# Kernel tuning notes

Hardware: AMD Instinct MI355X
Metric: run time of the kernel (lower is better)

## Reference

```python
import jax, jax.numpy as jnp
import numpy as np

B, T, D = 4, 4000, 1024
H = 8
DK = D // H          # key dim per head; value dim per head also DK (value_factor=1)
CHUNK = 500
EPS_LN = 1e-5
EPS_RMS = 1e-6


def rotate_every_two(x):
    x1 = x[..., ::2]
    x2 = x[..., 1::2]
    return jnp.stack((-x2, x1), axis=-1).reshape(x.shape)


def theta_shift(x, sin, cos):
    # x: [b,h,t,dk]; sin/cos: [t,dk]
    return x * cos + rotate_every_two(x) * sin


def rel_pos(slen, chunk_len, num_heads, key_dim):
    # RetNetRelPos(chunkwise_recurrent=True)
    angle = 1.0 / (10000 ** jnp.linspace(0.0, 1.0, key_dim // 2))
    angle = jnp.repeat(angle, 2)  # == unsqueeze(-1).repeat(1,2).flatten()
    decay = jnp.log(1.0 - 2.0 ** (-5.0 - jnp.arange(num_heads, dtype=jnp.float32)))
    index = jnp.arange(slen, dtype=jnp.float32)
    sin = jnp.sin(index[:, None] * angle[None, :])  # [t,dk]
    cos = jnp.cos(index[:, None] * angle[None, :])
    bi = jnp.arange(chunk_len, dtype=jnp.float32)
    tril = jnp.tril(jnp.ones((chunk_len, chunk_len), bool))
    diff = bi[:, None] - bi[None, :]
    mask = jnp.where(tril[None], jnp.exp(decay[:, None, None] * diff[None]), 0.0)  # [H,C,C]
    last_row = mask[:, -1]                                            # [H,C]
    value_inner_decay = (last_row / last_row.sum(-1, keepdims=True))[:, :, None]  # [H,C,1]
    scale = jnp.sqrt(mask.sum(-1, keepdims=True))                     # [H,C,1]
    inner_mask = mask / scale
    cross_decay = jnp.exp(decay * chunk_len)[:, None, None]           # [H,1,1]
    qid = jnp.exp(decay[:, None] * (bi + 1.0))[:, :, None]            # [H,C,1]
    query_inner_decay = qid / (scale / last_row.sum(-1)[:, None, None])
    return (sin, cos), (inner_mask, cross_decay, query_inner_decay, value_inner_decay)


def retention_chunkwise(qr, kr, v, inner):
    mask, cross_decay, query_inner_decay, value_inner_decay = inner
    b, t = v.shape[0], v.shape[1]
    C = mask.shape[1]
    n = t // C
    h, dk = qr.shape[1], qr.shape[3]
    dv = v.shape[2] // h
    # [b,h,t,dk] -> [b,n,h,C,dk]
    qr = qr.transpose(0, 2, 1, 3).reshape(b, n, C, h, dk).transpose(0, 1, 3, 2, 4)
    kr = kr.transpose(0, 2, 1, 3).reshape(b, n, C, h, dk).transpose(0, 1, 3, 2, 4)
    v = v.reshape(b, n, C, h, dv).transpose(0, 1, 3, 2, 4)  # [b,n,h,C,dv]

    qk = jnp.einsum('bnhcd,bnhed->bnhce', qr, kr) * mask  # [b,n,h,C,C]
    inner_scale = jnp.clip(jnp.abs(jax.lax.stop_gradient(qk)).sum(-1, keepdims=True), 1.0, None)
    qk = qk / inner_scale
    inner_output = jnp.einsum('bnhce,bnhed->bnhcd', qk, v)  # [b,n,h,C,dv]

    kv = jnp.einsum('bnhck,bnhcv->bnhkv', kr, v * value_inner_decay)  # [b,n,h,dk,dv]

    def step(carry, kv_i):
        kv_state, kv_scale = carry
        out = (kv_state / kv_scale, kv_scale)
        new_state = kv_state * cross_decay + kv_i
        sg = jnp.abs(jax.lax.stop_gradient(new_state)).sum(-2, keepdims=True).max(-1, keepdims=True)
        return (new_state, jnp.clip(sg, 1.0, None)), out

    init = (jnp.zeros((b, h, dk, dv), v.dtype), jnp.ones((b, h, 1, 1), v.dtype))
    _, (kv_rec, cross_scale) = jax.lax.scan(step, init, jnp.moveaxis(kv, 1, 0))
    kv_rec = jnp.moveaxis(kv_rec, 0, 1)            # [b,n,h,dk,dv]
    cross_scale = jnp.moveaxis(cross_scale, 0, 1)  # [b,n,h,1,1]

    all_scale = jnp.maximum(inner_scale, cross_scale)
    cross_output = jnp.einsum('bnhcd,bnhdv->bnhcv', qr * query_inner_decay, kv_rec)
    output = inner_output / (all_scale / inner_scale) + cross_output / (all_scale / cross_scale)
    return output.transpose(0, 1, 3, 2, 4).reshape(b, t, h, dv)  # [b,t,h,dv]


def setup_inputs() -> dict:
    key = jax.random.key(0)
    ks = jax.random.split(key, 6)
    s = 0.02
    return {
        'inputs': jax.random.normal(ks[0], (B, T, D), jnp.float32),
        'ln_gamma': jnp.ones((D,), jnp.float32),
        'ln_beta': jnp.zeros((D,), jnp.float32),
        'Wq': jax.random.normal(ks[1], (D, D), jnp.float32) * s,
        'Wk': jax.random.normal(ks[2], (D, D), jnp.float32) * s,
        'Wv': jax.random.normal(ks[3], (D, D), jnp.float32) * s,
        'Wg': jax.random.normal(ks[4], (D, D), jnp.float32) * s,
        'Wo': jax.random.normal(ks[5], (D, D), jnp.float32) * s,
    }


def reference(inputs, ln_gamma, ln_beta, Wq, Wk, Wv, Wg, Wo):
    b, t, d = inputs.shape
    # pre-LayerNorm
    mu = inputs.mean(-1, keepdims=True)
    var = ((inputs - mu) ** 2).mean(-1, keepdims=True)
    x = (inputs - mu) / jnp.sqrt(var + EPS_LN) * ln_gamma + ln_beta

    (sin, cos), inner = rel_pos(t, CHUNK, H, DK)

    q = (x @ Wq).reshape(b, t, H, DK).transpose(0, 2, 1, 3)
    k = (x @ Wk * (DK ** -0.5)).reshape(b, t, H, DK).transpose(0, 2, 1, 3)
    v = x @ Wv
    g = x @ Wg

    qr = theta_shift(q, sin, cos)
    kr = theta_shift(k, sin, cos)

    out = retention_chunkwise(qr, kr, v, inner)  # [b,t,H,dv]
    # group norm: per-head RMSNorm without affine
    out = out * jax.lax.rsqrt(jnp.mean(out ** 2, -1, keepdims=True) + EPS_RMS)
    out = out.reshape(b, t, H * DK)
    out = jax.nn.silu(g) * out
    return out @ Wo  # dropout is identity in eval
```

## Files before the change

### kernel.cpp

```cpp
#include <hip/hip_runtime.h>
#include <hip/hip_bf16.h>


typedef __attribute__((ext_vector_type(4))) float f32x4;
typedef __attribute__((ext_vector_type(8))) short s16x8;

#define DEV static __device__ __forceinline__

DEV float bfu(ushort u){ union{uint i; float f;} x; x.i=((uint)u)<<16; return x.f; }
DEV float bflo(uint w){ union{uint i; float f;} x; x.i=w<<16; return x.f; }
DEV float bfhi(uint w){ union{uint i; float f;} x; x.i=w&0xffff0000u; return x.f; }
DEV ushort f2bf(float f){ union{float f; uint u;} x; x.f=f; uint r = x.u + 0x7fffu + ((x.u>>16)&1u); return (ushort)(r>>16); }
DEV uint pack2(float lo, float hi){ return ((uint)f2bf(hi)<<16) | (uint)f2bf(lo); }
DEV void unpack8(uint4 u, float* f){
  f[0]=bflo(u.x); f[1]=bfhi(u.x); f[2]=bflo(u.y); f[3]=bfhi(u.y);
  f[4]=bflo(u.z); f[5]=bfhi(u.z); f[6]=bflo(u.w); f[7]=bfhi(u.w);
}
DEV void cstore(float* C, size_t i, float v){ C[i]=v; }
DEV void cstore(ushort* C, size_t i, float v){ C[i]=f2bf(v); }

DEV void gload16(const ushort* g, ushort* l) {
  __builtin_amdgcn_global_load_lds((const __attribute__((address_space(1))) void*)g,
                                   (__attribute__((address_space(3))) void*)l, 16, 0, 0);
}

__global__ __launch_bounds__(256) void f2bf_t_kernel(const float* __restrict__ src,
                                                     ushort* __restrict__ dst) {
  __shared__ ushort t[64][72];
  int kt = blockIdx.x*64, nt = blockIdx.y*64;
  int tid = threadIdx.x;
  int r = tid>>2, c0 = (tid&3)*16;
  const float* s = src + (size_t)(kt+r)*1024 + nt + c0;
  #pragma unroll
  for (int j=0;j<16;j+=4) {
    float4 vv = *(const float4*)(s+j);
    t[r][c0+j]=f2bf(vv.x); t[r][c0+j+1]=f2bf(vv.y); t[r][c0+j+2]=f2bf(vv.z); t[r][c0+j+3]=f2bf(vv.w);
  }
  __syncthreads();
  union { uint4 u4[2]; ushort s16[16]; } tmp;
  #pragma unroll
  for (int j=0;j<16;j++) tmp.s16[j] = t[c0+j][r];
  ushort* d = dst + (size_t)(nt+r)*1024 + kt + c0;
  *(uint4*)(d)   = tmp.u4[0];
  *(uint4*)(d+8) = tmp.u4[1];
}

__global__ __launch_bounds__(256) void ln_kernel(const float* __restrict__ x,
                                                 const float* __restrict__ gamma,
                                                 const float* __restrict__ beta,
                                                 ushort* __restrict__ xo) {
  int row = blockIdx.x;
  int tid = threadIdx.x;
  const float* xr = x + (size_t)row*1024;
  float4 u = ((const float4*)xr)[tid];
  float s = u.x+u.y+u.z+u.w;
  float sq = u.x*u.x+u.y*u.y+u.z*u.z+u.w*u.w;
  #pragma unroll
  for (int o=32;o;o>>=1){ s += __shfl_xor(s,o); sq += __shfl_xor(sq,o); }
  __shared__ float red[8];
  int wv=tid>>6, ln=tid&63;
  if (ln==0){ red[wv]=s; red[4+wv]=sq; }
  __syncthreads();
  s = red[0]+red[1]+red[2]+red[3];
  sq = red[4]+red[5]+red[6]+red[7];
  float mu = s*(1.0f/1024.0f);
  float var = sq*(1.0f/1024.0f)-mu*mu;
  float inv = rsqrtf(var+1e-5f);
  float4 gg = ((const float4*)gamma)[tid];
  float4 bb = ((const float4*)beta)[tid];
  float o0=(u.x-mu)*inv*gg.x+bb.x;
  float o1=(u.y-mu)*inv*gg.y+bb.y;
  float o2=(u.z-mu)*inv*gg.z+bb.z;
  float o3=(u.w-mu)*inv*gg.w+bb.w;
  uint2 w; w.x=pack2(o0,o1); w.y=pack2(o2,o3);
  ((uint2*)(xo+(size_t)row*1024))[tid]=w;
}

__global__ __launch_bounds__(256) void sincos_kernel(float* __restrict__ sint, float* __restrict__ cost) {
  int idx = blockIdx.x*256+threadIdx.x;
  if (idx >= 4000*64) return;
  int t = idx>>6, i = idx&63;
  float ang = expf(-9.210340371976184f * (float)i * (1.0f/63.0f));
  float a = (float)t * ang;
  float sv = sinf(a), cv = cosf(a);
  sint[(size_t)t*128+2*i] = sv; sint[(size_t)t*128+2*i+1] = sv;
  cost[(size_t)t*128+2*i] = cv; cost[(size_t)t*128+2*i+1] = cv;
}

template<typename OutT>
__global__ __launch_bounds__(256) void gemm_bt(const ushort* __restrict__ A,
                                               const ushort* __restrict__ BT,
                                               OutT* __restrict__ C,
                                               int M, int N, int K) {
  __shared__ ushort As[128*32];
  __shared__ ushort Bs[128*32];
  int ny = N>>7;
  int cpx = ((M>>7)*ny)>>3;
  int wg = blockIdx.x;
  int orig = (wg&7)*cpx + (wg>>3);
  int bm = (orig>>3)*128, bn = (orig&7)*128;
  int tid = threadIdx.x;
  int w = tid>>6, l = tid&63;
  int wm = (w>>1)*64, wn = (w&1)*64;
  int rsel = l&15, ko = (l>>4)*8;
  f32x4 acc[4][4];
  #pragma unroll
  for (int i=0;i<4;i++)
    #pragma unroll
    for (int j=0;j<4;j++){ acc[i][j][0]=0; acc[i][j][1]=0; acc[i][j][2]=0; acc[i][j][3]=0; }
  const ushort* ap0 = A  + (size_t)(bm + w*32 + (l>>2))*K + (l&3)*8;
  const ushort* ap1 = ap0 + (size_t)16*K;
  const ushort* bp0 = BT + (size_t)(bn + w*32 + (l>>2))*K + (l&3)*8;
  const ushort* bp1 = bp0 + (size_t)16*K;
  ushort* abase = As + w*1024;
  ushort* bbase = Bs + w*1024;
  for (int kt=0; kt<K; kt+=32) {
    __syncthreads();
    gload16(ap0+kt, abase);
    gload16(ap1+kt, abase+512);
    gload16(bp0+kt, bbase);
    gload16(bp1+kt, bbase+512);
    __syncthreads();
    s16x8 af[4], bfr[4];
    #pragma unroll
    for (int mf=0;mf<4;mf++) af[mf]  = *(const s16x8*)&As[(wm+mf*16+rsel)*32 + ko];
    #pragma unroll
    for (int nf=0;nf<4;nf++) bfr[nf] = *(const s16x8*)&Bs[(wn+nf*16+rsel)*32 + ko];
    #pragma unroll
    for (int mf=0;mf<4;mf++)
      #pragma unroll
      for (int nf=0;nf<4;nf++)
        acc[mf][nf] = __builtin_amdgcn_mfma_f32_16x16x32_bf16(af[mf], bfr[nf], acc[mf][nf], 0,0,0);
  }
  int crow = bm+wm+(l>>4)*4;
  int ccol = bn+wn+(l&15);
  #pragma unroll
  for (int mf=0;mf<4;mf++)
    #pragma unroll
    for (int nf=0;nf<4;nf++)
      #pragma unroll
      for (int r2=0;r2<4;r2++)
        cstore(C, (size_t)(crow+mf*16+r2)*N + ccol+nf*16, acc[mf][nf][r2]);
}

__global__ __launch_bounds__(256) void rotary_kernel(ushort* __restrict__ q, ushort* __restrict__ k,
                                                     const float* __restrict__ sint,
                                                     const float* __restrict__ cost) {
  int idx = blockIdx.x*256+threadIdx.x;
  if (idx >= 16000*512) return;
  int row = idx>>9, cp = idx&511;
  int col = cp*2;
  int t = row - (row/4000)*4000;
  int d = col & 127;
  float c = cost[(size_t)t*128+d], s = sint[(size_t)t*128+d];
  uint* qp = (uint*)(q + (size_t)row*1024 + col);
  uint w = *qp;
  float q0=bflo(w), q1=bfhi(w);
  *qp = pack2(q0*c - q1*s, q1*c + q0*s);
  uint* kp = (uint*)(k + (size_t)row*1024 + col);
  w = *kp;
  float k0=bflo(w), k1=bfhi(w);
  const float sc = 0.08838834764831845f;
  *kp = pack2((k0*c - k1*s)*sc, (k1*c + k0*s)*sc);
}

__global__ __launch_bounds__(256) void kv_mfma(const ushort* __restrict__ kr,
                                               const ushort* __restrict__ v,
                                               float* __restrict__ kvp) {
  int bnh = blockIdx.x, half = blockIdx.y;
  int h = bnh&7, n=(bnh>>3)&7, b=bnh>>6;
  size_t base = (size_t)(b*4000+n*500)*1024 + h*128;
  float Dh = 1.0f - exp2f(-5.0f-(float)h);
  float decay = logf(Dh);
  float ls = (1.0f - expf(decay*500.0f))/(1.0f-Dh);
  float inv_ls = 1.0f/ls;
  __shared__ ushort kT[128*72];
  __shared__ ushort vT[128*72];
  int tid=threadIdx.x;
  int wv=tid>>6, l=tid&63, g=l>>4, c16=l&15;
  int srow=tid>>2, sc0=(tid&3)*32;
  int cbeg = half*250, cend = cbeg+250;
  f32x4 acc[2][8];
  #pragma unroll
  for (int i=0;i<2;i++)
    #pragma unroll
    for (int j=0;j<8;j++){ acc[i][j][0]=0; acc[i][j][1]=0; acc[i][j][2]=0; acc[i][j][3]=0; }
  for (int ct=cbeg; ct<cend; ct+=64) {
    if (ct!=cbeg) __syncthreads();
    int c = ct + srow;
    int cc = min(c, 499);
    const ushort* ks = kr + base + (size_t)cc*1024 + sc0;
    const ushort* vs = v  + base + (size_t)cc*1024 + sc0;
    float vid = (c < cend && c < 500) ? expf(decay*(float)(499-c))*inv_ls : 0.0f;
    #pragma unroll
    for (int j=0;j<4;j++) {
      union{uint4 u; ushort s[8];} tk; tk.u = *(const uint4*)(ks+j*8);
      uint4 vv = *(const uint4*)(vs+j*8);
      float vf[8]; unpack8(vv,vf);
      #pragma unroll
      for (int x=0;x<8;x++) {
        kT[(sc0+j*8+x)*72 + srow] = tk.s[x];
        vT[(sc0+j*8+x)*72 + srow] = f2bf(vf[x]*vid);
      }
    }
    __syncthreads();
    #pragma unroll
    for (int kc=0;kc<2;kc++) {
      s16x8 a0 = *(const s16x8*)&kT[(wv*32 +      c16)*72 + kc*32 + g*8];
      s16x8 a1 = *(const s16x8*)&kT[(wv*32 + 16 + c16)*72 + kc*32 + g*8];
      #pragma unroll
      for (int nf=0;nf<8;nf++) {
        s16x8 bb = *(const s16x8*)&vT[(nf*16 + c16)*72 + kc*32 + g*8];
        acc[0][nf] = __builtin_amdgcn_mfma_f32_16x16x32_bf16(a0, bb, acc[0][nf], 0,0,0);
        acc[1][nf] = __builtin_amdgcn_mfma_f32_16x16x32_bf16(a1, bb, acc[1][nf], 0,0,0);
      }
    }
  }
  float* outp = kvp + ((size_t)half*256 + bnh)*16384;
  #pragma unroll
  for (int mf=0;mf<2;mf++)
    #pragma unroll
    for (int nf=0;nf<8;nf++)
      #pragma unroll
      for (int reg=0;reg<4;reg++)
        outp[(size_t)(wv*32 + mf*16 + g*4 + reg)*128 + nf*16 + c16] = acc[mf][nf][reg];
}

__global__ __launch_bounds__(256) void scan_kernel(const float* __restrict__ kvp,
                                                   ushort* __restrict__ kvrecT,
                                                   float* __restrict__ crosssc) {
  int bh = blockIdx.x;
  int b = bh>>3, h = bh&7;
  float Dh = 1.0f - exp2f(-5.0f-(float)h);
  float decay = logf(Dh);
  float cd = expf(decay*500.0f);
  int tid=threadIdx.x;
  int vcol = tid&127, khalf = tid>>7;
  float st[64];
  #pragma unroll
  for (int i=0;i<64;i++) st[i]=0;
  float scale = 1.0f;
  __shared__ float colpart[2][128];
  __shared__ float sred[2];
  for (int n=0;n<8;n++) {
    int bnh = (b*8+n)*8+h;
    const float* s0 = kvp + (size_t)bnh*16384;
    const float* s1 = kvp + (size_t)(256+bnh)*16384;
    ushort* rec = kvrecT + (size_t)bnh*16384;
    float inv = 1.0f/scale;
    float cs = 0;
    #pragma unroll
    for (int i=0;i<64;i++) {
      int kk = khalf*64+i;
      rec[(size_t)vcol*128+kk] = f2bf(st[i]*inv);
      st[i] = st[i]*cd + s0[(size_t)kk*128+vcol] + s1[(size_t)kk*128+vcol];
      cs += fabsf(st[i]);
    }
    if (tid==0) crosssc[bnh] = scale;
    colpart[khalf][vcol] = cs;
    __syncthreads();
    if (tid<128) colpart[0][tid] += colpart[1][tid];
    __syncthreads();
    float m = (tid<128)? colpart[0][tid] : 0.0f;
    #pragma unroll
    for (int o=32;o;o>>=1) m = fmaxf(m,__shfl_xor(m,o));
    if (tid<128 && (tid&63)==0) sred[tid>>6]=m;
    __syncthreads();
    scale = fmaxf(fmaxf(sred[0],sred[1]),1.0f);
    __syncthreads();
  }
}

__global__ __launch_bounds__(256) void iout_mfma(const ushort* __restrict__ qr,
                                                 const ushort* __restrict__ kr,
                                                 const ushort* __restrict__ v,
                                                 const ushort* __restrict__ kvrecT,
                                                 const float* __restrict__ crosssc,
                                                 ushort* __restrict__ O) {
  int bnh = blockIdx.x, rt = blockIdx.y;
  int h = bnh&7, n=(bnh>>3)&7, b=bnh>>6;
  size_t base = (size_t)(b*4000+n*500)*1024 + h*128;
  float Dh = 1.0f - exp2f(-5.0f-(float)h);
  float decay = logf(Dh);

  __shared__ ushort sh[31232];
  ushort* qt = sh;
  ushort* kt = sh + 8704;
  ushort* vt = sh + 17408;
  ushort* pt = sh + 26624;
  ushort* kvt = sh + 8704;

  int tid = threadIdx.x;
  int wv = tid>>6, l = tid&63;
  int g = l>>4, c16 = l&15;
  int srow = tid>>2, sc0 = (tid&3)*32;

  {
    int gq = rt*64+srow; if (gq>499) gq=499;
    const ushort* src = qr + base + (size_t)gq*1024 + sc0;
    #pragma unroll
    for (int j=0;j<4;j++) *(uint4*)&qt[srow*136 + sc0 + j*8] = *(const uint4*)(src + j*8);
  }
  int r_base = rt*64 + wv*16 + g*4;
  float er[4];
  #pragma unroll
  for (int reg=0;reg<4;reg++) er[reg] = expf(decay*(float)(r_base+reg));

  f32x4 pv[8], cc[8];
  #pragma unroll
  for (int i=0;i<8;i++){
    #pragma unroll
    for (int j=0;j<4;j++){ pv[i][j]=0.0f; cc[i][j]=0.0f; }
  }
  float rowsum[4] = {0,0,0,0};
  __syncthreads();

  for (int et=0; et<=rt; et++) {
    if (et) __syncthreads();
    {
      int ge = et*64+srow; if (ge>499) ge=499;
      const ushort* ks = kr + base + (size_t)ge*1024 + sc0;
      const ushort* vs = v  + base + (size_t)ge*1024 + sc0;
      #pragma unroll
      for (int j=0;j<4;j++) {
        *(uint4*)&kt[srow*136 + sc0 + j*8] = *(const uint4*)(ks + j*8);
        union{uint4 u; ushort s[8];} tv; tv.u = *(const uint4*)(vs + j*8);
        #pragma unroll
        for (int x=0;x<8;x++) vt[(sc0+j*8+x)*72 + srow] = tv.s[x];
      }
    }
    __syncthreads();
    f32x4 S[4];
    #pragma unroll
    for (int i=0;i<4;i++){ S[i][0]=0; S[i][1]=0; S[i][2]=0; S[i][3]=0; }
    #pragma unroll
    for (int kc=0;kc<4;kc++) {
      s16x8 a = *(const s16x8*)&qt[(wv*16 + c16)*136 + kc*32 + g*8];
      #pragma unroll
      for (int ni=0;ni<4;ni++) {
        s16x8 bf2 = *(const s16x8*)&kt[(ni*16 + c16)*136 + kc*32 + g*8];
        S[ni] = __builtin_amdgcn_mfma_f32_16x16x32_bf16(a, bf2, S[ni], 0,0,0);
      }
    }
    #pragma unroll
    for (int ni=0;ni<4;ni++) {
      int e_rel = et*64 + ni*16 + c16;
      float ie = expf(-decay*(float)e_rel);
      #pragma unroll
      for (int reg=0;reg<4;reg++) {
        int rr = r_base + reg;
        float p = (e_rel <= rr) ? S[ni][reg]*er[reg]*ie : 0.0f;
        rowsum[reg] += fabsf(p);
        pt[(wv*16 + g*4 + reg)*72 + ni*16 + c16] = f2bf(p);
      }
    }
    #pragma unroll
    for (int kc=0;kc<2;kc++) {
      s16x8 pa = *(const s16x8*)&pt[(wv*16 + c16)*72 + kc*32 + g*8];
      #pragma unroll
      for (int nf=0;nf<8;nf++) {
        s16x8 vb = *(const s16x8*)&vt[(nf*16 + c16)*72 + kc*32 + g*8];
        pv[nf] = __builtin_amdgcn_mfma_f32_16x16x32_bf16(pa, vb, pv[nf], 0,0,0);
      }
    }
  }
  #pragma unroll
  for (int reg=0;reg<4;reg++) {
    float s = rowsum[reg];
    s += __shfl_xor(s,1); s += __shfl_xor(s,2); s += __shfl_xor(s,4); s += __shfl_xor(s,8);
    rowsum[reg] = s;
  }
  __syncthreads();
  {
    int r2 = tid>>1, c0 = (tid&1)*64;
    const ushort* src = kvrecT + (size_t)bnh*16384 + (size_t)r2*128 + c0;
    #pragma unroll
    for (int j=0;j<8;j++) *(uint4*)&kvt[r2*136 + c0 + j*8] = *(const uint4*)(src + j*8);
  }
  __syncthreads();
  #pragma unroll
  for (int kc=0;kc<4;kc++) {
    s16x8 a = *(const s16x8*)&qt[(wv*16 + c16)*136 + kc*32 + g*8];
    #pragma unroll
    for (int nf=0;nf<8;nf++) {
      s16x8 bb = *(const s16x8*)&kvt[(nf*16 + c16)*136 + kc*32 + g*8];
      cc[nf] = __builtin_amdgcn_mfma_f32_16x16x32_bf16(a, bb, cc[nf], 0,0,0);
    }
  }
  float cs = crosssc[bnh];
  float lsum = (1.0f-expf(decay*500.0f))/(1.0f-Dh);
  #pragma unroll
  for (int reg=0;reg<4;reg++) {
    int rr = r_base + reg;
    if (rr < 500) {
      float rs = (1.0f-expf(decay*(float)(rr+1)))/(1.0f-Dh);
      float rsr = rsqrtf(rs);
      float is = fmaxf(1.0f, rowsum[reg]*rsr);
      float all = fmaxf(is, cs);
      float qid = expf(decay*(float)(rr+1))*lsum*rsr;
      float fi = rsr/all;
      float fc = qid*(cs/all);
      ushort* dst = O + (size_t)(b*4000+n*500+rr)*1024 + h*128;
      #pragma unroll
      for (int nf=0;nf<8;nf++)
        dst[nf*16 + c16] = f2bf(pv[nf][reg]*fi + cc[nf][reg]*fc);
    }
  }
}

__global__ __launch_bounds__(256) void rms_silu_kernel(const ushort* __restrict__ O,
                                                       const ushort* __restrict__ g,
                                                       ushort* __restrict__ op) {
  int row = blockIdx.x, tid=threadIdx.x;
  int wave=tid>>6, lane=tid&63;
  const ushort* Orow = O + (size_t)row*1024;
  const ushort* grow = g + (size_t)row*1024;
  ushort* orow = op + (size_t)row*1024;
  for (int hh=0; hh<2; hh++) {
    int h = wave*2+hh;
    int c0 = h*128+lane, c1=c0+64;
    float a = bfu(Orow[c0]), b2 = bfu(Orow[c1]);
    float ss = a*a+b2*b2;
    #pragma unroll
    for (int o=32;o;o>>=1) ss += __shfl_xor(ss,o);
    float sc = rsqrtf(ss*(1.0f/128.0f)+1e-6f);
    float g0=bfu(grow[c0]), g1=bfu(grow[c1]);
    float s0 = g0/(1.0f+expf(-g0)), s1 = g1/(1.0f+expf(-g1));
    orow[c0] = f2bf(s0*a*sc);
    orow[c1] = f2bf(s1*b2*sc);
  }
}

extern "C" void kernel_launch(void* const* d_in, const int* in_sizes, int n_in,
                              void* d_out, int out_size, void* d_ws, size_t ws_size,
                              hipStream_t stream) {
  const float* x     = (const float*)d_in[0];
  const float* gamma = (const float*)d_in[1];
  const float* beta  = (const float*)d_in[2];
  const float* Wq    = (const float*)d_in[3];
  const float* Wk    = (const float*)d_in[4];
  const float* Wv    = (const float*)d_in[5];
  const float* Wg    = (const float*)d_in[6];
  const float* Wo    = (const float*)d_in[7];
  float* out = (float*)d_out;

  char* ws = (char*)d_ws;
  size_t off = 0;
  auto alloc = [&](size_t bytes)->void* { void* p = ws+off; off += (bytes+255)&~(size_t)255; return p; };
  const size_t BT1024 = (size_t)16000*1024;
  ushort* xln  = (ushort*)alloc(BT1024*2);
  ushort* q    = (ushort*)alloc(BT1024*2);
  ushort* k    = (ushort*)alloc(BT1024*2);
  ushort* v    = (ushort*)alloc(BT1024*2);
  ushort* g    = (ushort*)alloc(BT1024*2);
  ushort* O    = (ushort*)alloc(BT1024*2);
  ushort* WqT  = (ushort*)alloc((size_t)1024*1024*2);
  ushort* WkT  = (ushort*)alloc((size_t)1024*1024*2);
  ushort* WvT  = (ushort*)alloc((size_t)1024*1024*2);
  ushort* WgT  = (ushort*)alloc((size_t)1024*1024*2);
  ushort* WoT  = (ushort*)alloc((size_t)1024*1024*2);
  float* sint  = (float*)alloc((size_t)4000*128*4);
  float* cost  = (float*)alloc((size_t)4000*128*4);
  float* kvp   = (float*)alloc((size_t)512*16384*4);
  ushort* kvrecT=(ushort*)alloc((size_t)256*16384*2);
  float* crosssc = (float*)alloc(256*4);
  (void)ws_size; (void)in_sizes; (void)n_in; (void)out_size;

  ln_kernel<<<16000,256,0,stream>>>(x,gamma,beta,xln);
  sincos_kernel<<<1000,256,0,stream>>>(sint,cost);
  dim3 tt(16,16);
  f2bf_t_kernel<<<tt,256,0,stream>>>(Wq,WqT);
  f2bf_t_kernel<<<tt,256,0,stream>>>(Wk,WkT);
  f2bf_t_kernel<<<tt,256,0,stream>>>(Wv,WvT);
  f2bf_t_kernel<<<tt,256,0,stream>>>(Wg,WgT);
  f2bf_t_kernel<<<tt,256,0,stream>>>(Wo,WoT);

  gemm_bt<ushort><<<1000,256,0,stream>>>(xln,WqT,q,16000,1024,1024);
  gemm_bt<ushort><<<1000,256,0,stream>>>(xln,WkT,k,16000,1024,1024);
  gemm_bt<ushort><<<1000,256,0,stream>>>(xln,WvT,v,16000,1024,1024);
  gemm_bt<ushort><<<1000,256,0,stream>>>(xln,WgT,g,16000,1024,1024);

  rotary_kernel<<<32000,256,0,stream>>>(q,k,sint,cost);

  dim3 gkv(256,2);
  kv_mfma<<<gkv,256,0,stream>>>(k,v,kvp);
  scan_kernel<<<32,256,0,stream>>>(kvp,kvrecT,crosssc);

  dim3 gr(256,8);
  iout_mfma<<<gr,256,0,stream>>>(q,k,v,kvrecT,crosssc,O);

  ushort* opre = xln;
  rms_silu_kernel<<<16000,256,0,stream>>>(O,g,opre);
  gemm_bt<float><<<1000,256,0,stream>>>(opre,WoT,out,16000,1024,1024);
}
```

Before: 471.4 us.

## Double-buffer GEMM, pre-transpose K/V, fold decays into q/k, fuse RMS+SiLU

Several changes land together. The projection GEMM now double-buffers its LDS tiles so the next K-slice loads while MFMAs run. Rotary for K moves into a new kernel that also folds the per-position decay into q and k and writes transposed K/V copies. kv_mfma and iout_mfma use those copies through swizzled LDS loaded with global_load_lds. The RMSNorm and SiLU gating move into the retention output epilogue, which removes the O buffer and the separate rms_silu pass. Folding the decay as exp(-decay*c) into k can lose precision for large in-chunk offsets with bf16 storage.

Measured after the change: 478.6 us. No clear change (+1.5%).

```diff
diff --git a/kernel.cpp b/kernel.cpp
--- a/kernel.cpp
+++ b/kernel.cpp
@@ -92,8 +92,8 @@
                                                const ushort* __restrict__ BT,
                                                OutT* __restrict__ C,
                                                int M, int N, int K) {
-  __shared__ ushort As[128*32];
-  __shared__ ushort Bs[128*32];
+  __shared__ ushort As[8192];
+  __shared__ ushort Bs[8192];
   int ny = N>>7;
   int cpx = ((M>>7)*ny)>>3;
   int wg = blockIdx.x;
@@ -112,25 +112,33 @@
   const ushort* ap1 = ap0 + (size_t)16*K;
   const ushort* bp0 = BT + (size_t)(bn + w*32 + (l>>2))*K + (l&3)*8;
   const ushort* bp1 = bp0 + (size_t)16*K;
-  ushort* abase = As + w*1024;
-  ushort* bbase = Bs + w*1024;
+  {
+    ushort* ab = As + w*1024; ushort* bb = Bs + w*1024;
+    gload16(ap0, ab); gload16(ap1, ab+512);
+    gload16(bp0, bb); gload16(bp1, bb+512);
+  }
+  int cur = 0;
   for (int kt=0; kt<K; kt+=32) {
     __syncthreads();
-    gload16(ap0+kt, abase);
-    gload16(ap1+kt, abase+512);
-    gload16(bp0+kt, bbase);
-    gload16(bp1+kt, bbase+512);
-    __syncthreads();
+    if (kt+32 < K) {
+      int nb = cur^1;
+      ushort* ab = As + nb*4096 + w*1024; ushort* bb = Bs + nb*4096 + w*1024;
+      gload16(ap0+kt+32, ab); gload16(ap1+kt+32, ab+512);
+      gload16(bp0+kt+32, bb); gload16(bp1+kt+32, bb+512);
+    }
+    const ushort* Ac = As + cur*4096;
+    const ushort* Bc = Bs + cur*4096;
     s16x8 af[4], bfr[4];
     #pragma unroll
-    for (int mf=0;mf<4;mf++) af[mf]  = *(const s16x8*)&As[(wm+mf*16+rsel)*32 + ko];
-    #pragma unroll
-    for (int nf=0;nf<4;nf++) bfr[nf] = *(const s16x8*)&Bs[(wn+nf*16+rsel)*32 + ko];
+    for (int mf=0;mf<4;mf++) af[mf]  = *(const s16x8*)&Ac[(wm+mf*16+rsel)*32 + ko];
+    #pragma unroll
+    for (int nf=0;nf<4;nf++) bfr[nf] = *(const s16x8*)&Bc[(wn+nf*16+rsel)*32 + ko];
     #pragma unroll
     for (int mf=0;mf<4;mf++)
       #pragma unroll
       for (int nf=0;nf<4;nf++)
         acc[mf][nf] = __builtin_amdgcn_mfma_f32_16x16x32_bf16(af[mf], bfr[nf], acc[mf][nf], 0,0,0);
+    cur ^= 1;
   }
   int crow = bm+wm+(l>>4)*4;
   int ccol = bn+wn+(l&15);
@@ -143,87 +151,138 @@
         cstore(C, (size_t)(crow+mf*16+r2)*N + ccol+nf*16, acc[mf][nf][r2]);
 }
 
-__global__ __launch_bounds__(256) void rotary_kernel(ushort* __restrict__ q, ushort* __restrict__ k,
-                                                     const float* __restrict__ sint,
-                                                     const float* __restrict__ cost) {
+__global__ __launch_bounds__(256) void qrot_kernel(ushort* __restrict__ q,
+                                                   const float* __restrict__ sint,
+                                                   const float* __restrict__ cost) {
   int idx = blockIdx.x*256+threadIdx.x;
   if (idx >= 16000*512) return;
   int row = idx>>9, cp = idx&511;
   int col = cp*2;
   int t = row - (row/4000)*4000;
-  int d = col & 127;
+  int d = col & 127, h = col>>7;
+  int r_rel = t - (t/500)*500;
+  float decay = logf(1.0f - exp2f(-5.0f-(float)h));
+  float qs = expf(decay*(float)r_rel);
   float c = cost[(size_t)t*128+d], s = sint[(size_t)t*128+d];
   uint* qp = (uint*)(q + (size_t)row*1024 + col);
   uint w = *qp;
   float q0=bflo(w), q1=bfhi(w);
-  *qp = pack2(q0*c - q1*s, q1*c + q0*s);
-  uint* kp = (uint*)(k + (size_t)row*1024 + col);
-  w = *kp;
-  float k0=bflo(w), k1=bfhi(w);
-  const float sc = 0.08838834764831845f;
-  *kp = pack2((k0*c - k1*s)*sc, (k1*c + k0*s)*sc);
-}
-
-__global__ __launch_bounds__(256) void kv_mfma(const ushort* __restrict__ kr,
-                                               const ushort* __restrict__ v,
-                                               float* __restrict__ kvp) {
-  int bnh = blockIdx.x, half = blockIdx.y;
+  *qp = pack2((q0*c - q1*s)*qs, (q1*c + q0*s)*qs);
+}
+
+__global__ __launch_bounds__(256) void kvT_kernel(ushort* __restrict__ k,
+                                                  const ushort* __restrict__ v,
+                                                  ushort* __restrict__ kT,
+                                                  ushort* __restrict__ vT,
+                                                  const float* __restrict__ sint,
+                                                  const float* __restrict__ cost) {
+  int bnh = blockIdx.x, ct = blockIdx.y;
   int h = bnh&7, n=(bnh>>3)&7, b=bnh>>6;
   size_t base = (size_t)(b*4000+n*500)*1024 + h*128;
-  float Dh = 1.0f - exp2f(-5.0f-(float)h);
-  float decay = logf(Dh);
-  float ls = (1.0f - expf(decay*500.0f))/(1.0f-Dh);
-  float inv_ls = 1.0f/ls;
-  __shared__ ushort kT[128*72];
-  __shared__ ushort vT[128*72];
+  float decay = logf(1.0f - exp2f(-5.0f-(float)h));
+  __shared__ ushort ktl[64][136];
+  __shared__ ushort vtl[64][136];
+  int tid = threadIdx.x;
+  int srow = tid>>2, sc0 = (tid&3)*32;
+  int c = ct*64 + srow;
+  if (c < 500) {
+    int t = n*500 + c;
+    float ksc = expf(-decay*(float)c) * 0.08838834764831845f;
+    ushort* kp = k + base + (size_t)c*1024 + sc0;
+    const ushort* vp = v + base + (size_t)c*1024 + sc0;
+    #pragma unroll
+    for (int j=0;j<4;j++) {
+      uint4 kw = *(const uint4*)(kp+j*8);
+      float kf[8]; unpack8(kw,kf);
+      uint4 ko4;
+      uint* kou = (uint*)&ko4;
+      #pragma unroll
+      for (int p=0;p<4;p++) {
+        int d = sc0+j*8+2*p;
+        float cc = cost[(size_t)t*128+d], ss = sint[(size_t)t*128+d];
+        float r0 = (kf[2*p]*cc - kf[2*p+1]*ss)*ksc;
+        float r1 = (kf[2*p+1]*cc + kf[2*p]*ss)*ksc;
+        kou[p] = pack2(r0,r1);
+      }
+      *(uint4*)&ktl[srow][sc0+j*8] = ko4;
+      *(uint4*)(kp+j*8) = ko4;
+      *(uint4*)&vtl[srow][sc0+j*8] = *(const uint4*)(vp+j*8);
+    }
+  } else {
+    uint4 z; z.x=0;z.y=0;z.z=0;z.w=0;
+    #pragma unroll
+    for (int j=0;j<4;j++){ *(uint4*)&ktl[srow][sc0+j*8]=z; *(uint4*)&vtl[srow][sc0+j*8]=z; }
+  }
+  __syncthreads();
+  int d = tid>>1, ch = (tid&1)*32;
+  union{uint4 u4[4]; ushort s[32];} pk, pv_;
+  #pragma unroll
+  for (int j=0;j<32;j++){ pk.s[j] = ktl[ch+j][d]; pv_.s[j] = vtl[ch+j][d]; }
+  ushort* kd = kT + (size_t)bnh*65536 + (size_t)d*512 + ct*64 + ch;
+  ushort* vd = vT + (size_t)bnh*65536 + (size_t)d*512 + ct*64 + ch;
+  #pragma unroll
+  for (int j=0;j<4;j++){ *(uint4*)(kd+j*8) = pk.u4[j]; *(uint4*)(vd+j*8) = pv_.u4[j]; }
+}
+
+__global__ __launch_bounds__(256) void kv_mfma(const ushort* __restrict__ kT,
+                                               const ushort* __restrict__ vT,
+                                               float* __restrict__ kvp) {
+  int bnh = blockIdx.x;
+  __shared__ ushort sh2[16384];
   int tid=threadIdx.x;
   int wv=tid>>6, l=tid&63, g=l>>4, c16=l&15;
-  int srow=tid>>2, sc0=(tid&3)*32;
-  int cbeg = half*250, cend = cbeg+250;
-  f32x4 acc[2][8];
-  #pragma unroll
-  for (int i=0;i<2;i++)
-    #pragma unroll
-    for (int j=0;j<8;j++){ acc[i][j][0]=0; acc[i][j][1]=0; acc[i][j][2]=0; acc[i][j][3]=0; }
-  for (int ct=cbeg; ct<cend; ct+=64) {
-    if (ct!=cbeg) __syncthreads();
-    int c = ct + srow;
-    int cc = min(c, 499);
-    const ushort* ks = kr + base + (size_t)cc*1024 + sc0;
-    const ushort* vs = v  + base + (size_t)cc*1024 + sc0;
-    float vid = (c < cend && c < 500) ? expf(decay*(float)(499-c))*inv_ls : 0.0f;
-    #pragma unroll
-    for (int j=0;j<4;j++) {
-      union{uint4 u; ushort s[8];} tk; tk.u = *(const uint4*)(ks+j*8);
-      uint4 vv = *(const uint4*)(vs+j*8);
-      float vf[8]; unpack8(vv,vf);
-      #pragma unroll
-      for (int x=0;x<8;x++) {
-        kT[(sc0+j*8+x)*72 + srow] = tk.s[x];
-        vT[(sc0+j*8+x)*72 + srow] = f2bf(vf[x]*vid);
-      }
+  int wr = wv>>1, wc = wv&1;
+  int ri[4], ro[4];
+  #pragma unroll
+  for (int jj=0;jj<4;jj++){
+    int i = wv*256 + jj*64 + l;
+    ri[jj] = i>>3;
+    ro[jj] = (((i&7)*16) ^ ((ri[jj]&7)<<4))>>1;
+  }
+  const ushort* kbase = kT + (size_t)bnh*65536;
+  const ushort* vbase = vT + (size_t)bnh*65536;
+  f32x4 acc[4][4];
+  #pragma unroll
+  for (int i=0;i<4;i++)
+    #pragma unroll
+    for (int j=0;j<4;j++){ acc[i][j][0]=0; acc[i][j][1]=0; acc[i][j][2]=0; acc[i][j][3]=0; }
+  for (int ctep=0; ctep<8; ctep++) {
+    int cb = ctep*64;
+    __syncthreads();
+    #pragma unroll
+    for (int jj=0;jj<4;jj++){
+      gload16(kbase + (size_t)ri[jj]*512 + cb + ro[jj], (ushort*)((char*)sh2 + wv*4096 + jj*1024));
+      gload16(vbase + (size_t)ri[jj]*512 + cb + ro[jj], (ushort*)((char*)sh2 + 16384 + wv*4096 + jj*1024));
     }
     __syncthreads();
     #pragma unroll
     for (int kc=0;kc<2;kc++) {
-      s16x8 a0 = *(const s16x8*)&kT[(wv*32 +      c16)*72 + kc*32 + g*8];
-      s16x8 a1 = *(const s16x8*)&kT[(wv*32 + 16 + c16)*72 + kc*32 + g*8];
-      #pragma unroll
-      for (int nf=0;nf<8;nf++) {
-        s16x8 bb = *(const s16x8*)&vT[(nf*16 + c16)*72 + kc*32 + g*8];
-        acc[0][nf] = __builtin_amdgcn_mfma_f32_16x16x32_bf16(a0, bb, acc[0][nf], 0,0,0);
-        acc[1][nf] = __builtin_amdgcn_mfma_f32_16x16x32_bf16(a1, bb, acc[1][nf], 0,0,0);
-      }
-    }
-  }
-  float* outp = kvp + ((size_t)half*256 + bnh)*16384;
-  #pragma unroll
-  for (int mf=0;mf<2;mf++)
-    #pragma unroll
-    for (int nf=0;nf<8;nf++)
+      s16x8 af[4], bf2[4];
+      #pragma unroll
+      for (int mf=0;mf<4;mf++){
+        int row = wr*64+mf*16+c16;
+        af[mf] = *(const s16x8*)((const char*)sh2 + row*128 + ((((kc*32+g*8)*2)) ^ ((row&7)<<4)));
+      }
+      #pragma unroll
+      for (int nf=0;nf<4;nf++){
+        int row = wc*64+nf*16+c16;
+        bf2[nf] = *(const s16x8*)((const char*)sh2 + 16384 + row*128 + ((((kc*32+g*8)*2)) ^ ((row&7)<<4)));
+      }
+      #pragma unroll
+      for (int mf=0;mf<4;mf++)
+        #pragma unroll
+        for (int nf=0;nf<4;nf++)
+          acc[mf][nf] = __builtin_amdgcn_mfma_f32_16x16x32_bf16(af[mf], bf2[nf], acc[mf][nf], 0,0,0);
+    }
+  }
+  float* outp = kvp + (size_t)bnh*16384;
+  #pragma unroll
+  for (int mf=0;mf<4;mf++)
+    #pragma unroll
+    for (int nf=0;nf<4;nf++)
       #pragma unroll
       for (int reg=0;reg<4;reg++)
-        outp[(size_t)(wv*32 + mf*16 + g*4 + reg)*128 + nf*16 + c16] = acc[mf][nf][reg];
+        outp[(size_t)(wr*64+mf*16+g*4+reg)*128 + wc*64+nf*16+c16] = acc[mf][nf][reg];
 }
 
 __global__ __launch_bounds__(256) void scan_kernel(const float* __restrict__ kvp,
@@ -234,6 +293,8 @@
   float Dh = 1.0f - exp2f(-5.0f-(float)h);
   float decay = logf(Dh);
   float cd = expf(decay*500.0f);
+  float ls = (1.0f - expf(decay*500.0f))/(1.0f-Dh);
+  float cst = expf(decay*499.0f)/ls;
   int tid=threadIdx.x;
   int vcol = tid&127, khalf = tid>>7;
   float st[64];
@@ -244,8 +305,7 @@
   __shared__ float sred[2];
   for (int n=0;n<8;n++) {
     int bnh = (b*8+n)*8+h;
-    const float* s0 = kvp + (size_t)bnh*16384;
-    const float* s1 = kvp + (size_t)(256+bnh)*16384;
+    const float* src = kvp + (size_t)bnh*16384;
     ushort* rec = kvrecT + (size_t)bnh*16384;
     float inv = 1.0f/scale;
     float cs = 0;
@@ -253,7 +313,7 @@
     for (int i=0;i<64;i++) {
       int kk = khalf*64+i;
       rec[(size_t)vcol*128+kk] = f2bf(st[i]*inv);
-      st[i] = st[i]*cd + s0[(size_t)kk*128+vcol] + s1[(size_t)kk*128+vcol];
+      st[i] = st[i]*cd + cst*src[(size_t)kk*128+vcol];
       cs += fabsf(st[i]);
     }
     if (tid==0) crosssc[bnh] = scale;
@@ -271,40 +331,39 @@
   }
 }
 
-__global__ __launch_bounds__(256) void iout_mfma(const ushort* __restrict__ qr,
-                                                 const ushort* __restrict__ kr,
-                                                 const ushort* __restrict__ v,
-                                                 const ushort* __restrict__ kvrecT,
-                                                 const float* __restrict__ crosssc,
-                                                 ushort* __restrict__ O) {
+__global__ __launch_bounds__(256,4) void iout_mfma(const ushort* __restrict__ qr,
+                                                   const ushort* __restrict__ kr,
+                                                   const ushort* __restrict__ vT,
+                                                   const ushort* __restrict__ kvrecT,
+                                                   const float* __restrict__ crosssc,
+                                                   const ushort* __restrict__ gbuf,
+                                                   ushort* __restrict__ opre) {
   int bnh = blockIdx.x, rt = blockIdx.y;
   int h = bnh&7, n=(bnh>>3)&7, b=bnh>>6;
   size_t base = (size_t)(b*4000+n*500)*1024 + h*128;
   float Dh = 1.0f - exp2f(-5.0f-(float)h);
   float decay = logf(Dh);
-
-  __shared__ ushort sh[31232];
-  ushort* qt = sh;
-  ushort* kt = sh + 8704;
-  ushort* vt = sh + 17408;
-  ushort* pt = sh + 26624;
-  ushort* kvt = sh + 8704;
-
+  __shared__ ushort sh[20480];
+  char* shb = (char*)sh;
   int tid = threadIdx.x;
   int wv = tid>>6, l = tid&63;
   int g = l>>4, c16 = l&15;
-  int srow = tid>>2, sc0 = (tid&3)*32;
-
-  {
-    int gq = rt*64+srow; if (gq>499) gq=499;
-    const ushort* src = qr + base + (size_t)gq*1024 + sc0;
-    #pragma unroll
-    for (int j=0;j<4;j++) *(uint4*)&qt[srow*136 + sc0 + j*8] = *(const uint4*)(src + j*8);
-  }
   int r_base = rt*64 + wv*16 + g*4;
-  float er[4];
-  #pragma unroll
-  for (int reg=0;reg<4;reg++) er[reg] = expf(decay*(float)(r_base+reg));
+
+  int qrow = rt*64 + wv*16 + c16; if (qrow>499) qrow=499;
+  s16x8 aq[4];
+  #pragma unroll
+  for (int kc=0;kc<4;kc++)
+    aq[kc] = *(const s16x8*)(qr + base + (size_t)qrow*1024 + kc*32 + g*8);
+
+  int ktrow[4], ktofs[4], vtrow[4], vtofs[4];
+  #pragma unroll
+  for (int jj=0;jj<4;jj++){
+    int i = wv*256 + jj*64 + l;
+    int r_ = i>>4;  ktrow[jj]=r_;  ktofs[jj] = (((i&15)*16) ^ ((r_&7)<<4))>>1;
+    int r2_ = i>>3; vtrow[jj]=r2_; vtofs[jj] = (((i&7)*16) ^ ((r2_&7)<<4))>>1;
+  }
+  const ushort* vTb = vT + (size_t)bnh*65536;
 
   f32x4 pv[8], cc[8];
   #pragma unroll
@@ -313,21 +372,14 @@
     for (int j=0;j<4;j++){ pv[i][j]=0.0f; cc[i][j]=0.0f; }
   }
   float rowsum[4] = {0,0,0,0};
-  __syncthreads();
 
   for (int et=0; et<=rt; et++) {
-    if (et) __syncthreads();
-    {
-      int ge = et*64+srow; if (ge>499) ge=499;
-      const ushort* ks = kr + base + (size_t)ge*1024 + sc0;
-      const ushort* vs = v  + base + (size_t)ge*1024 + sc0;
-      #pragma unroll
-      for (int j=0;j<4;j++) {
-        *(uint4*)&kt[srow*136 + sc0 + j*8] = *(const uint4*)(ks + j*8);
-        union{uint4 u; ushort s[8];} tv; tv.u = *(const uint4*)(vs + j*8);
-        #pragma unroll
-        for (int x=0;x<8;x++) vt[(sc0+j*8+x)*72 + srow] = tv.s[x];
-      }
+    __syncthreads();
+    #pragma unroll
+    for (int jj=0;jj<4;jj++){
+      int gr = et*64 + ktrow[jj]; if (gr>499) gr=499;
+      gload16(kr + base + (size_t)gr*1024 + ktofs[jj], (ushort*)(shb + wv*4096 + jj*1024));
+      gload16(vTb + (size_t)vtrow[jj]*512 + et*64 + vtofs[jj], (ushort*)(shb + 16384 + wv*4096 + jj*1024));
     }
     __syncthreads();
     f32x4 S[4];
@@ -335,31 +387,34 @@
     for (int i=0;i<4;i++){ S[i][0]=0; S[i][1]=0; S[i][2]=0; S[i][3]=0; }
     #pragma unroll
     for (int kc=0;kc<4;kc++) {
-      s16x8 a = *(const s16x8*)&qt[(wv*16 + c16)*136 + kc*32 + g*8];
       #pragma unroll
       for (int ni=0;ni<4;ni++) {
-        s16x8 bf2 = *(const s16x8*)&kt[(ni*16 + c16)*136 + kc*32 + g*8];
-        S[ni] = __builtin_amdgcn_mfma_f32_16x16x32_bf16(a, bf2, S[ni], 0,0,0);
-      }
-    }
+        int krow = ni*16+c16;
+        s16x8 bf = *(const s16x8*)(shb + krow*256 + ((((kc*32+g*8)*2)) ^ ((krow&7)<<4)));
+        S[ni] = __builtin_amdgcn_mfma_f32_16x16x32_bf16(aq[kc], bf, S[ni], 0,0,0);
+      }
+    }
+    bool diag = (et==rt);
     #pragma unroll
     for (int ni=0;ni<4;ni++) {
       int e_rel = et*64 + ni*16 + c16;
-      float ie = expf(-decay*(float)e_rel);
       #pragma unroll
       for (int reg=0;reg<4;reg++) {
-        int rr = r_base + reg;
-        float p = (e_rel <= rr) ? S[ni][reg]*er[reg]*ie : 0.0f;
+        float p = S[ni][reg];
+        if (diag && e_rel > r_base+reg) p = 0.0f;
         rowsum[reg] += fabsf(p);
-        pt[(wv*16 + g*4 + reg)*72 + ni*16 + c16] = f2bf(p);
+        int prow = wv*16 + g*4 + reg;
+        *(ushort*)(shb + 32768 + prow*128 + (((ni*16+c16)*2) ^ ((prow&7)<<4))) = f2bf(p);
       }
     }
     #pragma unroll
     for (int kc=0;kc<2;kc++) {
-      s16x8 pa = *(const s16x8*)&pt[(wv*16 + c16)*72 + kc*32 + g*8];
+      int prow = wv*16 + c16;
+      s16x8 pa = *(const s16x8*)(shb + 32768 + prow*128 + ((((kc*32+g*8)*2)) ^ ((prow&7)<<4)));
       #pragma unroll
       for (int nf=0;nf<8;nf++) {
-        s16x8 vb = *(const s16x8*)&vt[(nf*16 + c16)*72 + kc*32 + g*8];
+        int vrow = nf*16+c16;
+        s16x8 vb = *(const s16x8*)(shb + 16384 + vrow*128 + ((((kc*32+g*8)*2)) ^ ((vrow&7)<<4)));
         pv[nf] = __builtin_amdgcn_mfma_f32_16x16x32_bf16(pa, vb, pv[nf], 0,0,0);
       }
     }
@@ -371,24 +426,26 @@
     rowsum[reg] = s;
   }
   __syncthreads();
-  {
-    int r2 = tid>>1, c0 = (tid&1)*64;
-    const ushort* src = kvrecT + (size_t)bnh*16384 + (size_t)r2*128 + c0;
-    #pragma unroll
-    for (int j=0;j<8;j++) *(uint4*)&kvt[r2*136 + c0 + j*8] = *(const uint4*)(src + j*8);
+  #pragma unroll
+  for (int jj=0;jj<8;jj++){
+    int i = wv*512 + jj*64 + l;
+    int r_ = i>>4;
+    int ofs = (((i&15)*16) ^ ((r_&7)<<4))>>1;
+    gload16(kvrecT + (size_t)bnh*16384 + (size_t)r_*128 + ofs, (ushort*)(shb + wv*8192 + jj*1024));
   }
   __syncthreads();
   #pragma unroll
   for (int kc=0;kc<4;kc++) {
-    s16x8 a = *(const s16x8*)&qt[(wv*16 + c16)*136 + kc*32 + g*8];
     #pragma unroll
     for (int nf=0;nf<8;nf++) {
-      s16x8 bb = *(const s16x8*)&kvt[(nf*16 + c16)*136 + kc*32 + g*8];
-      cc[nf] = __builtin_amdgcn_mfma_f32_16x16x32_bf16(a, bb, cc[nf], 0,0,0);
+      int krow = nf*16+c16;
+      s16x8 bb = *(const s16x8*)(shb + krow*256 + ((((kc*32+g*8)*2)) ^ ((krow&7)<<4)));
+      cc[nf] = __builtin_amdgcn_mfma_f32_16x16x32_bf16(aq[kc], bb, cc[nf], 0,0,0);
     }
   }
   float cs = crosssc[bnh];
   float lsum = (1.0f-expf(decay*500.0f))/(1.0f-Dh);
+  float ed = expf(decay);
   #pragma unroll
   for (int reg=0;reg<4;reg++) {
     int rr = r_base + reg;
@@ -397,37 +454,22 @@
       float rsr = rsqrtf(rs);
       float is = fmaxf(1.0f, rowsum[reg]*rsr);
       float all = fmaxf(is, cs);
-      float qid = expf(decay*(float)(rr+1))*lsum*rsr;
+      float qid = ed*lsum*rsr;
       float fi = rsr/all;
       float fc = qid*(cs/all);
-      ushort* dst = O + (size_t)(b*4000+n*500+rr)*1024 + h*128;
-      #pragma unroll
-      for (int nf=0;nf<8;nf++)
-        dst[nf*16 + c16] = f2bf(pv[nf][reg]*fi + cc[nf][reg]*fc);
-    }
-  }
-}
-
-__global__ __launch_bounds__(256) void rms_silu_kernel(const ushort* __restrict__ O,
-                                                       const ushort* __restrict__ g,
-                                                       ushort* __restrict__ op) {
-  int row = blockIdx.x, tid=threadIdx.x;
-  int wave=tid>>6, lane=tid&63;
-  const ushort* Orow = O + (size_t)row*1024;
-  const ushort* grow = g + (size_t)row*1024;
-  ushort* orow = op + (size_t)row*1024;
-  for (int hh=0; hh<2; hh++) {
-    int h = wave*2+hh;
-    int c0 = h*128+lane, c1=c0+64;
-    float a = bfu(Orow[c0]), b2 = bfu(Orow[c1]);
-    float ss = a*a+b2*b2;
-    #pragma unroll
-    for (int o=32;o;o>>=1) ss += __shfl_xor(ss,o);
-    float sc = rsqrtf(ss*(1.0f/128.0f)+1e-6f);
-    float g0=bfu(grow[c0]), g1=bfu(grow[c1]);
-    float s0 = g0/(1.0f+expf(-g0)), s1 = g1/(1.0f+expf(-g1));
-    orow[c0] = f2bf(s0*a*sc);
-    orow[c1] = f2bf(s1*b2*sc);
+      float o[8]; float ssq = 0.0f;
+      #pragma unroll
+      for (int nf=0;nf<8;nf++){ o[nf] = pv[nf][reg]*fi + cc[nf][reg]*fc; ssq += o[nf]*o[nf]; }
+      ssq += __shfl_xor(ssq,1); ssq += __shfl_xor(ssq,2); ssq += __shfl_xor(ssq,4); ssq += __shfl_xor(ssq,8);
+      float rmss = rsqrtf(ssq*(1.0f/128.0f)+1e-6f);
+      size_t rowoff = (size_t)(b*4000+n*500+rr)*1024 + h*128;
+      #pragma unroll
+      for (int nf=0;nf<8;nf++){
+        float gv = bfu(gbuf[rowoff + nf*16 + c16]);
+        float sg = gv/(1.0f+expf(-gv));
+        opre[rowoff + nf*16 + c16] = f2bf(sg*o[nf]*rmss);
+      }
+    }
   }
 }
 
@@ -453,7 +495,6 @@
   ushort* k    = (ushort*)alloc(BT1024*2);
   ushort* v    = (ushort*)alloc(BT1024*2);
   ushort* g    = (ushort*)alloc(BT1024*2);
-  ushort* O    = (ushort*)alloc(BT1024*2);
   ushort* WqT  = (ushort*)alloc((size_t)1024*1024*2);
   ushort* WkT  = (ushort*)alloc((size_t)1024*1024*2);
   ushort* WvT  = (ushort*)alloc((size_t)1024*1024*2);
@@ -461,7 +502,8 @@
   ushort* WoT  = (ushort*)alloc((size_t)1024*1024*2);
   float* sint  = (float*)alloc((size_t)4000*128*4);
   float* cost  = (float*)alloc((size_t)4000*128*4);
-  float* kvp   = (float*)alloc((size_t)512*16384*4);
+  ushort* kT   = (ushort*)alloc((size_t)256*65536*2);
+  ushort* vT   = (ushort*)alloc((size_t)256*65536*2);
   ushort* kvrecT=(ushort*)alloc((size_t)256*16384*2);
   float* crosssc = (float*)alloc(256*4);
   (void)ws_size; (void)in_sizes; (void)n_in; (void)out_size;
@@ -480,16 +522,17 @@
   gemm_bt<ushort><<<1000,256,0,stream>>>(xln,WvT,v,16000,1024,1024);
   gemm_bt<ushort><<<1000,256,0,stream>>>(xln,WgT,g,16000,1024,1024);
 
-  rotary_kernel<<<32000,256,0,stream>>>(q,k,sint,cost);
-
-  dim3 gkv(256,2);
-  kv_mfma<<<gkv,256,0,stream>>>(k,v,kvp);
+  qrot_kernel<<<32000,256,0,stream>>>(q,sint,cost);
+  dim3 gkt(256,8);
+  kvT_kernel<<<gkt,256,0,stream>>>(k,v,kT,vT,sint,cost);
+
+  float* kvp = (float*)xln;
+  kv_mfma<<<256,256,0,stream>>>(kT,vT,kvp);
   scan_kernel<<<32,256,0,stream>>>(kvp,kvrecT,crosssc);
 
+  ushort* opre = xln;
   dim3 gr(256,8);
-  iout_mfma<<<gr,256,0,stream>>>(q,k,v,kvrecT,crosssc,O);
-
-  ushort* opre = xln;
-  rms_silu_kernel<<<16000,256,0,stream>>>(O,g,opre);
+  iout_mfma<<<gr,256,0,stream>>>(q,k,vT,kvrecT,crosssc,g,opre);
+
   gemm_bt<float><<<1000,256,0,stream>>>(opre,WoT,out,16000,1024,1024);
 }
```
